# Kernel optimization log

Measured on AMD Instinct MI355X. Metric: run time of the kernel, lower is better.

## Reference

```python
import jax, jax.numpy as jnp
import numpy as np

EPS = 1e-6
B, T, D = 8, 4096, 512


def setup_inputs() -> dict:
    key = jax.random.key(0)
    ks = jax.random.split(key, 8)
    s = 1.0 / np.sqrt(D)
    return {
        "summarization": jax.random.normal(ks[0], (B, D), jnp.float32),
        "decoder_output": jax.random.normal(ks[1], (B, T, D), jnp.float32),
        "W_hist": jax.random.normal(ks[2], (D, D), jnp.float32) * s,
        "b_hist": jnp.zeros((D,), jnp.float32),
        "W1": jax.random.normal(ks[3], (D, D), jnp.float32) * s,
        "W2": jax.random.normal(ks[4], (D, D), jnp.float32) * s,
        "W_out": jax.random.normal(ks[5], (D, D), jnp.float32) * s,
        "b_out": jnp.zeros((D,), jnp.float32),
        "gamma": jnp.ones((D,), jnp.float32),
        "beta": jnp.zeros((D,), jnp.float32),
    }


def reference(summarization, decoder_output, W_hist, b_hist, W1, W2, W_out, b_out, gamma, beta):
    # Causal running mean: equivalent to tril-mask bmm / row-count, but O(T).
    tgt_len = decoder_output.shape[1]
    counts = jnp.arange(1, tgt_len + 1, dtype=decoder_output.dtype)[None, :, None]
    history = jnp.cumsum(decoder_output, axis=1) / counts            # [B,T,D]
    history = jnp.tanh(history @ W_hist + b_hist)                    # history_linear + tanh
    # TransformMinus: linear1(summ) - linear2(history), then linear_out + tanh
    summ_proj = (summarization @ W1)[:, None, :]                     # [B,1,D] broadcasts over T
    out = summ_proj - history @ W2
    future = jnp.tanh(out @ W_out + b_out)
    # LayerPostprocessing (eval: dropout = identity): LayerNorm(future + decoder_output)
    x = future + decoder_output
    mu = jnp.mean(x, axis=-1, keepdims=True)
    var = jnp.mean(jnp.square(x - mu), axis=-1, keepdims=True)
    return (x - mu) / jnp.sqrt(var + EPS) * gamma + beta
```

## Files before the change

kernel.cpp:

```cpp
#include <hip/hip_runtime.h>
#include <hip/hip_bf16.h>
#include <stdint.h>
#include <stddef.h>

#define DEV static __device__ __forceinline__

typedef __attribute__((ext_vector_type(8))) short short8;
typedef __attribute__((ext_vector_type(4))) float floatx4;

constexpr int Tn = 4096, Dn = 512;
constexpr int NC = 128, CTm = 32;

union U8s { uint4 u4; unsigned short us[8]; };
union U4f { float4 f4; float f[4]; };
union U4s { uint2 u2; unsigned short us[4]; };

DEV float b2f(unsigned short u) {
  union { unsigned int i; float f; } c; c.i = ((unsigned int)u) << 16; return c.f;
}
DEV unsigned short f2b(float f) {
  union { float f; unsigned int u; } c; c.f = f;
  unsigned int r = c.u + 0x7fffu + ((c.u >> 16) & 1u);
  return (unsigned short)(r >> 16);
}
DEV float fast_tanh(float x) {
  float e = __expf(2.0f * x);
  return 1.0f - 2.0f / (e + 1.0f);
}

typedef __attribute__((address_space(1))) void GVOID;
typedef __attribute__((address_space(3))) void LVOID;
DEV void async16(const unsigned short* g, unsigned short* l) {
  __builtin_amdgcn_global_load_lds((GVOID*)g, (LVOID*)l, 16, 0, 0);
}

__global__ void k_scan_partial(const float* __restrict__ dec, float* __restrict__ part) {
  int idx = blockIdx.x * 256 + threadIdx.x;
  int d4 = idx & 127;
  int c  = (idx >> 7) & (NC - 1);
  int b  = idx >> 14;
  const float* p = dec + ((size_t)b * Tn + (size_t)c * CTm) * Dn + d4 * 4;
  float s[4] = {0,0,0,0};
#pragma unroll 4
  for (int i = 0; i < CTm; ++i) {
    U4f v; v.f4 = *(const float4*)(p + (size_t)i * Dn);
#pragma unroll
    for (int j = 0; j < 4; ++j) s[j] += v.f[j];
  }
  float* o = part + ((size_t)(b * NC + c)) * Dn + d4 * 4;
#pragma unroll
  for (int j = 0; j < 4; ++j) o[j] = s[j];
}

__global__ void k_scan_prefix(float* __restrict__ part) {
  int idx = blockIdx.x * 256 + threadIdx.x;
  int d = idx & 511; int b = idx >> 9;
  float* p = part + (size_t)b * NC * Dn + d;
  float run = 0.f;
#pragma unroll 4
  for (int c = 0; c < NC; ++c) {
    float v = p[(size_t)c * Dn];
    p[(size_t)c * Dn] = run;
    run += v;
  }
}

__global__ void k_scan_apply(const float* __restrict__ dec,
                             const float* __restrict__ part,
                             unsigned short* __restrict__ M) {
  int idx = blockIdx.x * 256 + threadIdx.x;
  int d4 = idx & 127;
  int c  = (idx >> 7) & (NC - 1);
  int b  = idx >> 14;
  size_t rbase = (size_t)b * Tn + (size_t)c * CTm;
  const float* pp = part + ((size_t)(b * NC + c)) * Dn + d4 * 4;
  float s[4];
#pragma unroll
  for (int j = 0; j < 4; ++j) s[j] = pp[j];
  int t0 = c * CTm;
  for (int i = 0; i < CTm; ++i) {
    U4f v; v.f4 = *(const float4*)(dec + (rbase + i) * Dn + d4 * 4);
    U4s o;
    float inv = 1.0f / (float)(t0 + i + 1);
#pragma unroll
    for (int j = 0; j < 4; ++j) { s[j] += v.f[j]; o.us[j] = f2b(s[j] * inv); }
    *(uint2*)(M + (rbase + i) * Dn + d4 * 4) = o.u2;
  }
}

__global__ void k_svec(const float* __restrict__ summ,
                       const unsigned short* __restrict__ W1WoT,
                       const float* __restrict__ bo,
                       float* __restrict__ spo) {
  int widx = blockIdx.x * 4 + (threadIdx.x >> 6);
  int lane = threadIdx.x & 63;
  int n = widx & 511; int b = widx >> 9;
  U8s w8; w8.u4 = *(const uint4*)(W1WoT + (size_t)n * Dn + lane * 8);
  U4f s0, s1;
  s0.f4 = *(const float4*)(summ + (size_t)b * Dn + lane * 8);
  s1.f4 = *(const float4*)(summ + (size_t)b * Dn + lane * 8 + 4);
  float acc = 0.f;
#pragma unroll
  for (int j = 0; j < 4; ++j) acc += s0.f[j] * b2f(w8.us[j]);
#pragma unroll
  for (int j = 0; j < 4; ++j) acc += s1.f[j] * b2f(w8.us[j + 4]);
#pragma unroll
  for (int o = 32; o > 0; o >>= 1) acc += __shfl_xor(acc, o, 64);
  if (lane == 0) spo[(size_t)b * Dn + n] = acc + bo[n];
}

__global__ void k_transpose512(const float* __restrict__ in,
                               unsigned short* __restrict__ out) {
  __shared__ float t[64][65];
  int bx = blockIdx.x & 7, by = blockIdx.x >> 3;
  int n0 = bx * 64, k0 = by * 64;
#pragma unroll
  for (int l = 0; l < 16; ++l) {
    int lin = l * 256 + threadIdx.x;
    int r = lin >> 6, c = lin & 63;
    t[r][c] = in[(size_t)(k0 + r) * 512 + n0 + c];
  }
  __syncthreads();
#pragma unroll
  for (int l = 0; l < 16; ++l) {
    int lin = l * 256 + threadIdx.x;
    int r = lin >> 6, c = lin & 63;
    out[(size_t)(n0 + r) * 512 + k0 + c] = f2b(t[c][r]);
  }
}

__global__ void k_convert512(const float* __restrict__ in, unsigned short* __restrict__ out) {
  int idx = blockIdx.x * 256 + threadIdx.x;
  U4f v; v.f4 = *(const float4*)(in + (size_t)idx * 4);
  U4s o;
#pragma unroll
  for (int j = 0; j < 4; ++j) o.us[j] = f2b(v.f[j]);
  *(uint2*)(out + (size_t)idx * 4) = o.u2;
}

template<int EPI>
__global__ __launch_bounds__(256, 2)
void k_gemm(const unsigned short* __restrict__ A, const unsigned short* __restrict__ BT,
            unsigned short* __restrict__ C, const float* __restrict__ bias,
            const float* __restrict__ sproj) {
  __shared__ alignas(16) unsigned short sA[128 * 64];
  __shared__ alignas(16) unsigned short sB[128 * 64];
  const int tid  = threadIdx.x;
  const int lane = tid & 63;
  const int w    = tid >> 6;
  const int m0   = blockIdx.x * 128;
  const int n0   = blockIdx.y * 128;
  const int wm   = (w >> 1) * 64;
  const int wn   = (w & 1) * 64;
  const int rs   = lane & 15;
  const int quad = lane >> 4;

  floatx4 acc[4][4];
#pragma unroll
  for (int i = 0; i < 4; ++i)
#pragma unroll
    for (int j = 0; j < 4; ++j) acc[i][j] = (floatx4){0.f, 0.f, 0.f, 0.f};

  for (int kt = 0; kt < 512; kt += 64) {
#pragma unroll
    for (int l = 0; l < 4; ++l) {
      int ch = l * 256 + tid;
      int r = ch >> 3, kc = ch & 7;
      async16(A  + (size_t)(m0 + r) * 512 + kt + kc * 8, sA + (size_t)ch * 8);
      async16(BT + (size_t)(n0 + r) * 512 + kt + kc * 8, sB + (size_t)ch * 8);
    }
    asm volatile("s_waitcnt vmcnt(0)" ::: "memory");
    __syncthreads();

#pragma unroll
    for (int kk = 0; kk < 2; ++kk) {
      const int kb = kk * 32 + quad * 8;
      short8 af[4], bfr[4];
#pragma unroll
      for (int i = 0; i < 4; ++i)
        af[i] = *(const short8*)(sA + (size_t)(wm + i * 16 + rs) * 64 + kb);
#pragma unroll
      for (int j = 0; j < 4; ++j)
        bfr[j] = *(const short8*)(sB + (size_t)(wn + j * 16 + rs) * 64 + kb);
#pragma unroll
      for (int i = 0; i < 4; ++i)
#pragma unroll
        for (int j = 0; j < 4; ++j)
          acc[i][j] = __builtin_amdgcn_mfma_f32_16x16x32_bf16(af[i], bfr[j], acc[i][j], 0, 0, 0);
    }
    __syncthreads();
  }

#pragma unroll
  for (int i = 0; i < 4; ++i) {
#pragma unroll
    for (int j = 0; j < 4; ++j) {
      const int colg = n0 + wn + j * 16 + rs;
#pragma unroll
      for (int r = 0; r < 4; ++r) {
        const int rowg = m0 + wm + i * 16 + quad * 4 + r;
        float v = acc[i][j][r];
        if constexpr (EPI == 0)      v = fast_tanh(v + bias[colg]);
        else if constexpr (EPI == 3) v = fast_tanh(sproj[(rowg >> 12) * Dn + colg] - v);
        C[(size_t)rowg * 512 + colg] = f2b(v);
      }
    }
  }
}

__global__ void k_ln(const unsigned short* __restrict__ F, const float* __restrict__ dec,
                     const float* __restrict__ gamma, const float* __restrict__ beta,
                     float* __restrict__ out) {
  int row  = blockIdx.x * 4 + (threadIdx.x >> 6);
  int lane = threadIdx.x & 63;
  size_t base = (size_t)row * Dn + lane * 8;
  U8s f8; f8.u4 = *(const uint4*)(F + base);
  U4f d0, d1; d0.f4 = *(const float4*)(dec + base); d1.f4 = *(const float4*)(dec + base + 4);
  float x[8]; float s = 0.f, sq = 0.f;
#pragma unroll
  for (int j = 0; j < 8; ++j) {
    float dv = (j < 4) ? d0.f[j] : d1.f[j - 4];
    x[j] = b2f(f8.us[j]) + dv; s += x[j]; sq += x[j] * x[j];
  }
#pragma unroll
  for (int o = 32; o > 0; o >>= 1) { s += __shfl_xor(s, o, 64); sq += __shfl_xor(sq, o, 64); }
  float mu   = s * (1.0f / 512.0f);
  float var  = sq * (1.0f / 512.0f) - mu * mu;
  float rstd = rsqrtf(var + 1e-6f);
  U4f g0, g1, b0, b1, o0, o1;
  g0.f4 = *(const float4*)(gamma + lane * 8); g1.f4 = *(const float4*)(gamma + lane * 8 + 4);
  b0.f4 = *(const float4*)(beta  + lane * 8); b1.f4 = *(const float4*)(beta  + lane * 8 + 4);
#pragma unroll
  for (int j = 0; j < 8; ++j) {
    float g = (j < 4) ? g0.f[j] : g1.f[j - 4];
    float b = (j < 4) ? b0.f[j] : b1.f[j - 4];
    float v = (x[j] - mu) * rstd * g + b;
    if (j < 4) o0.f[j] = v; else o1.f[j - 4] = v;
  }
  *(float4*)(out + base) = o0.f4;
  *(float4*)(out + base + 4) = o1.f4;
}

extern "C" void kernel_launch(void* const* d_in, const int* in_sizes, int n_in,
                              void* d_out, int out_size, void* d_ws, size_t ws_size,
                              hipStream_t stream) {
  (void)in_sizes; (void)n_in; (void)out_size; (void)ws_size;
  const float* summ = (const float*)d_in[0];
  const float* dec  = (const float*)d_in[1];
  const float* Wh   = (const float*)d_in[2];
  const float* bh   = (const float*)d_in[3];
  const float* W1   = (const float*)d_in[4];
  const float* W2   = (const float*)d_in[5];
  const float* Wo   = (const float*)d_in[6];
  const float* bo   = (const float*)d_in[7];
  const float* gam  = (const float*)d_in[8];
  const float* bet  = (const float*)d_in[9];
  float* out = (float*)d_out;

  char* ws = (char*)d_ws;
  unsigned short* Mbuf  = (unsigned short*)(ws);
  unsigned short* Hbuf  = (unsigned short*)(ws + 33554432);
  float*          part  = (float*)(ws + 67108864);
  float*          spo   = (float*)(ws + 69206016);
  unsigned short* WhT   = (unsigned short*)(ws + 69238784);
  unsigned short* WoT   = (unsigned short*)(ws + 69763072);
  unsigned short* W2b   = (unsigned short*)(ws + 70287360);
  unsigned short* W2WoT = (unsigned short*)(ws + 70811648);
  unsigned short* W1b   = (unsigned short*)(ws + 71335936);
  unsigned short* W1WoT = (unsigned short*)(ws + 71860224);

  k_transpose512<<<64, 256, 0, stream>>>(Wh, WhT);
  k_transpose512<<<64, 256, 0, stream>>>(Wo, WoT);
  k_convert512<<<256, 256, 0, stream>>>(W2, W2b);
  k_convert512<<<256, 256, 0, stream>>>(W1, W1b);
  k_gemm<2><<<dim3(4, 4), 256, 0, stream>>>(WoT, W2b, W2WoT, nullptr, nullptr);
  k_gemm<2><<<dim3(4, 4), 256, 0, stream>>>(WoT, W1b, W1WoT, nullptr, nullptr);

  k_scan_partial<<<512, 256, 0, stream>>>(dec, part);
  k_scan_prefix<<<16, 256, 0, stream>>>(part);
  k_scan_apply<<<512, 256, 0, stream>>>(dec, part, Mbuf);

  k_svec<<<1024, 256, 0, stream>>>(summ, W1WoT, bo, spo);

  k_gemm<0><<<dim3(256, 4), 256, 0, stream>>>(Mbuf, WhT, Hbuf, bh, nullptr);
  k_gemm<3><<<dim3(256, 4), 256, 0, stream>>>(Hbuf, W2WoT, Mbuf, nullptr, spo);

  k_ln<<<8192, 256, 0, stream>>>(Mbuf, dec, gam, bet, out);
}
```

Before: 276.6 us.

## Merge weight-prep launches and fold scan prefix into apply kernel

Merges the two transposes and two conversions into a single weight-prep kernel and the two weight-product GEMMs into one launch using a z-dimension. Removes the separate serial prefix kernel, so each scan-apply thread now sums the preceding chunk partials itself and handles 8 columns with 128-bit stores. This cuts the launch count and removes a low-parallelism serial kernel. In exchange it adds redundant partial-sum reads (up to 127 chunks per thread) and halves the scan-apply grid.

```diff
diff --git a/kernel.cpp b/kernel.cpp
--- a/kernel.cpp
+++ b/kernel.cpp
@@ -52,39 +52,35 @@
   for (int j = 0; j < 4; ++j) o[j] = s[j];
 }
 
-__global__ void k_scan_prefix(float* __restrict__ part) {
-  int idx = blockIdx.x * 256 + threadIdx.x;
-  int d = idx & 511; int b = idx >> 9;
-  float* p = part + (size_t)b * NC * Dn + d;
-  float run = 0.f;
-#pragma unroll 4
-  for (int c = 0; c < NC; ++c) {
-    float v = p[(size_t)c * Dn];
-    p[(size_t)c * Dn] = run;
-    run += v;
-  }
-}
-
 __global__ void k_scan_apply(const float* __restrict__ dec,
                              const float* __restrict__ part,
                              unsigned short* __restrict__ M) {
   int idx = blockIdx.x * 256 + threadIdx.x;
-  int d4 = idx & 127;
-  int c  = (idx >> 7) & (NC - 1);
-  int b  = idx >> 14;
+  int d8 = idx & 63;
+  int c  = (idx >> 6) & (NC - 1);
+  int b  = idx >> 13;
   size_t rbase = (size_t)b * Tn + (size_t)c * CTm;
-  const float* pp = part + ((size_t)(b * NC + c)) * Dn + d4 * 4;
-  float s[4];
-#pragma unroll
-  for (int j = 0; j < 4; ++j) s[j] = pp[j];
+  float s[8] = {0,0,0,0,0,0,0,0};
+  const float* pb = part + (size_t)b * NC * Dn + d8 * 8;
+  for (int cc = 0; cc < c; ++cc) {
+    U4f p0, p1;
+    p0.f4 = *(const float4*)(pb + (size_t)cc * Dn);
+    p1.f4 = *(const float4*)(pb + (size_t)cc * Dn + 4);
+#pragma unroll
+    for (int j = 0; j < 4; ++j) { s[j] += p0.f[j]; s[j + 4] += p1.f[j]; }
+  }
   int t0 = c * CTm;
   for (int i = 0; i < CTm; ++i) {
-    U4f v; v.f4 = *(const float4*)(dec + (rbase + i) * Dn + d4 * 4);
-    U4s o;
+    U4f v0, v1; U8s o;
+    v0.f4 = *(const float4*)(dec + (rbase + i) * Dn + d8 * 8);
+    v1.f4 = *(const float4*)(dec + (rbase + i) * Dn + d8 * 8 + 4);
     float inv = 1.0f / (float)(t0 + i + 1);
 #pragma unroll
-    for (int j = 0; j < 4; ++j) { s[j] += v.f[j]; o.us[j] = f2b(s[j] * inv); }
-    *(uint2*)(M + (rbase + i) * Dn + d4 * 4) = o.u2;
+    for (int j = 0; j < 4; ++j) {
+      s[j] += v0.f[j];     o.us[j]     = f2b(s[j] * inv);
+      s[j + 4] += v1.f[j]; o.us[j + 4] = f2b(s[j + 4] * inv);
+    }
+    *(uint4*)(M + (rbase + i) * Dn + d8 * 8) = o.u4;
   }
 }
 
@@ -109,47 +105,55 @@
   if (lane == 0) spo[(size_t)b * Dn + n] = acc + bo[n];
 }
 
-__global__ void k_transpose512(const float* __restrict__ in,
-                               unsigned short* __restrict__ out) {
-  __shared__ float t[64][65];
-  int bx = blockIdx.x & 7, by = blockIdx.x >> 3;
-  int n0 = bx * 64, k0 = by * 64;
-#pragma unroll
-  for (int l = 0; l < 16; ++l) {
-    int lin = l * 256 + threadIdx.x;
-    int r = lin >> 6, c = lin & 63;
-    t[r][c] = in[(size_t)(k0 + r) * 512 + n0 + c];
-  }
-  __syncthreads();
-#pragma unroll
-  for (int l = 0; l < 16; ++l) {
-    int lin = l * 256 + threadIdx.x;
-    int r = lin >> 6, c = lin & 63;
-    out[(size_t)(n0 + r) * 512 + k0 + c] = f2b(t[c][r]);
-  }
-}
-
-__global__ void k_convert512(const float* __restrict__ in, unsigned short* __restrict__ out) {
-  int idx = blockIdx.x * 256 + threadIdx.x;
-  U4f v; v.f4 = *(const float4*)(in + (size_t)idx * 4);
-  U4s o;
-#pragma unroll
-  for (int j = 0; j < 4; ++j) o.us[j] = f2b(v.f[j]);
-  *(uint2*)(out + (size_t)idx * 4) = o.u2;
+__global__ void k_wprep(const float* __restrict__ Wh, const float* __restrict__ Wo,
+                        const float* __restrict__ W1, const float* __restrict__ W2,
+                        unsigned short* __restrict__ WhT, unsigned short* __restrict__ WoT,
+                        unsigned short* __restrict__ W1b, unsigned short* __restrict__ W2b) {
+  int blk = blockIdx.x;
+  if (blk < 128) {
+    const float* in = (blk < 64) ? Wh : Wo;
+    unsigned short* out = (blk < 64) ? WhT : WoT;
+    int lb = blk & 63;
+    __shared__ float t[64][65];
+    int n0 = (lb & 7) * 64, k0 = (lb >> 3) * 64;
+#pragma unroll
+    for (int l = 0; l < 16; ++l) {
+      int lin = l * 256 + threadIdx.x;
+      int r = lin >> 6, c = lin & 63;
+      t[r][c] = in[(size_t)(k0 + r) * 512 + n0 + c];
+    }
+    __syncthreads();
+#pragma unroll
+    for (int l = 0; l < 16; ++l) {
+      int lin = l * 256 + threadIdx.x;
+      int r = lin >> 6, c = lin & 63;
+      out[(size_t)(n0 + r) * 512 + k0 + c] = f2b(t[c][r]);
+    }
+  } else {
+    const float* in = (blk < 160) ? W1 : W2;
+    unsigned short* out = (blk < 160) ? W1b : W2b;
+    int lb = (blk - 128) & 31;
+    size_t base = ((size_t)lb * 256 + threadIdx.x) * 32;
+#pragma unroll
+    for (int l = 0; l < 8; ++l) {
+      U4f v; v.f4 = *(const float4*)(in + base + l * 4);
+      U4s o;
+#pragma unroll
+      for (int j = 0; j < 4; ++j) o.us[j] = f2b(v.f[j]);
+      *(uint2*)(out + base + l * 4) = o.u2;
+    }
+  }
 }
 
 template<int EPI>
-__global__ __launch_bounds__(256, 2)
-void k_gemm(const unsigned short* __restrict__ A, const unsigned short* __restrict__ BT,
-            unsigned short* __restrict__ C, const float* __restrict__ bias,
-            const float* __restrict__ sproj) {
+DEV void gemm_core(const unsigned short* __restrict__ A, const unsigned short* __restrict__ BT,
+                   unsigned short* __restrict__ C, const float* __restrict__ bias,
+                   const float* __restrict__ sproj, int m0, int n0) {
   __shared__ alignas(16) unsigned short sA[128 * 64];
   __shared__ alignas(16) unsigned short sB[128 * 64];
   const int tid  = threadIdx.x;
   const int lane = tid & 63;
   const int w    = tid >> 6;
-  const int m0   = blockIdx.x * 128;
-  const int n0   = blockIdx.y * 128;
   const int wm   = (w >> 1) * 64;
   const int wn   = (w & 1) * 64;
   const int rs   = lane & 15;
@@ -206,6 +210,23 @@
       }
     }
   }
+}
+
+template<int EPI>
+__global__ __launch_bounds__(256, 2)
+void k_gemm(const unsigned short* __restrict__ A, const unsigned short* __restrict__ BT,
+            unsigned short* __restrict__ C, const float* __restrict__ bias,
+            const float* __restrict__ sproj) {
+  gemm_core<EPI>(A, BT, C, bias, sproj, blockIdx.x * 128, blockIdx.y * 128);
+}
+
+__global__ __launch_bounds__(256, 2)
+void k_wgemm(const unsigned short* __restrict__ WoT,
+             const unsigned short* __restrict__ W2b, const unsigned short* __restrict__ W1b,
+             unsigned short* __restrict__ W2WoT, unsigned short* __restrict__ W1WoT) {
+  const unsigned short* BT = blockIdx.z ? W1b : W2b;
+  unsigned short* C = blockIdx.z ? W1WoT : W2WoT;
+  gemm_core<2>(WoT, BT, C, nullptr, nullptr, blockIdx.x * 128, blockIdx.y * 128);
 }
 
 __global__ void k_ln(const unsigned short* __restrict__ F, const float* __restrict__ dec,
@@ -269,18 +290,14 @@
   unsigned short* W1b   = (unsigned short*)(ws + 71335936);
   unsigned short* W1WoT = (unsigned short*)(ws + 71860224);
 
-  k_transpose512<<<64, 256, 0, stream>>>(Wh, WhT);
-  k_transpose512<<<64, 256, 0, stream>>>(Wo, WoT);
-  k_convert512<<<256, 256, 0, stream>>>(W2, W2b);
-  k_convert512<<<256, 256, 0, stream>>>(W1, W1b);
-  k_gemm<2><<<dim3(4, 4), 256, 0, stream>>>(WoT, W2b, W2WoT, nullptr, nullptr);
-  k_gemm<2><<<dim3(4, 4), 256, 0, stream>>>(WoT, W1b, W1WoT, nullptr, nullptr);
-
   k_scan_partial<<<512, 256, 0, stream>>>(dec, part);
-  k_scan_prefix<<<16, 256, 0, stream>>>(part);
-  k_scan_apply<<<512, 256, 0, stream>>>(dec, part, Mbuf);
+
+  k_wprep<<<192, 256, 0, stream>>>(Wh, Wo, W1, W2, WhT, WoT, W1b, W2b);
+  k_wgemm<<<dim3(4, 4, 2), 256, 0, stream>>>(WoT, W2b, W1b, W2WoT, W1WoT);
 
   k_svec<<<1024, 256, 0, stream>>>(summ, W1WoT, bo, spo);
+
+  k_scan_apply<<<256, 256, 0, stream>>>(dec, part, Mbuf);
 
   k_gemm<0><<<dim3(256, 4), 256, 0, stream>>>(Mbuf, WhT, Hbuf, bh, nullptr);
   k_gemm<3><<<dim3(256, 4), 256, 0, stream>>>(Hbuf, W2WoT, Mbuf, nullptr, spo);
```

Result: faster. 265.4 us (-4.0%).
